# Kernel optimization log

Measured on AMD Instinct MI355X. Metric: run time of the kernel, lower is better.

Reference implementation:

```python
import jax, jax.numpy as jnp
import numpy as np

N_NODES = 50000
N_EDGES = 800000
IN_FT = 256
OUT_FT = 128


def setup_inputs() -> dict:
    key = jax.random.key(0)
    k_seq, k_src, k_dst, k_val, k_w = jax.random.split(key, 5)
    seq = jax.random.normal(k_seq, (N_NODES, IN_FT), dtype=jnp.float32)
    edge_src = jax.random.randint(k_src, (N_EDGES,), 0, N_NODES, dtype=jnp.int64)
    edge_dst = jax.random.randint(k_dst, (N_EDGES,), 0, N_NODES, dtype=jnp.int64)
    edge_val = jax.random.uniform(k_val, (N_EDGES,), dtype=jnp.float32)
    # xavier_uniform for Linear(in_ft, out_ft): limit = sqrt(6/(in+out))
    limit = float(np.sqrt(6.0 / (IN_FT + OUT_FT)))
    W = jax.random.uniform(k_w, (OUT_FT, IN_FT), minval=-limit, maxval=limit, dtype=jnp.float32)
    bias = jnp.zeros((OUT_FT,), dtype=jnp.float32)
    prelu_a = jnp.full((1,), 0.25, dtype=jnp.float32)  # nn.PReLU default slope
    return {"seq": seq, "edge_src": edge_src, "edge_dst": edge_dst,
            "edge_val": edge_val, "W": W, "bias": bias, "prelu_a": prelu_a}


def reference(seq, edge_src, edge_dst, edge_val, W, bias, prelu_a):
    # seq_fts = fc(seq): [N, out_ft]
    seq_fts = jnp.einsum('ni,oi->no', seq, W)
    # sparse spmm: out[dst] += val * seq_fts[src]
    msgs = seq_fts[edge_src] * edge_val[:, None]          # [E, out_ft]
    out = jax.ops.segment_sum(msgs, edge_dst, num_segments=seq.shape[0])
    out = out + bias                                       # bias add
    # PReLU with learnable slope a
    return jnp.where(out >= 0, out, prelu_a * out)
```

## Files before the change

kernel.cpp:

```cpp
#include <hip/hip_runtime.h>
#include <hip/hip_bf16.h>

#define N_NODES 50000
#define N_EDGES 800000
#define IN_FT 256
#define OUT_FT 128

typedef __bf16 bf16;
typedef __attribute__((ext_vector_type(8))) __bf16 bf16x8;
typedef __attribute__((ext_vector_type(4))) float floatx4;

static __device__ inline unsigned short f2bf_bits(float f) {
    unsigned u = __float_as_uint(f);
    return (unsigned short)((u + 0x7FFFu + ((u >> 16) & 1u)) >> 16);
}

__global__ __launch_bounds__(256) void k_wconv(const float* __restrict__ W,
                                               unsigned short* __restrict__ Wb) {
    int i = blockIdx.x * 256 + threadIdx.x;
    float4 v = ((const float4*)W)[i];
    ushort4 o;
    o.x = f2bf_bits(v.x); o.y = f2bf_bits(v.y);
    o.z = f2bf_bits(v.z); o.w = f2bf_bits(v.w);
    ((ushort4*)Wb)[i] = o;
}

#define WP 264
#define GM 128

__global__ __launch_bounds__(512) void k_gemm(const float* __restrict__ seq,
                                              const unsigned short* __restrict__ Wb,
                                              unsigned short* __restrict__ seq_fts) {
    __shared__ bf16 Wlds[128 * WP];
    const int t = threadIdx.x;

    {
        const int row = t >> 2, c0 = (t & 3) * 64;
        const unsigned short* src = Wb + row * IN_FT + c0;
        bf16* dst = Wlds + row * WP + c0;
#pragma unroll
        for (int c = 0; c < 8; ++c)
            *(uint4*)(dst + c * 8) = *(const uint4*)(src + c * 8);
    }

    const int lane = t & 63;
    const int wave = t >> 6;
    const int quad = lane >> 4;
    const int l16  = lane & 15;

    int arow = blockIdx.x * GM + wave * 16 + l16;
    if (arow >= N_NODES) arow = 0;
    const float* ap = seq + (size_t)arow * IN_FT + quad * 8;
    bf16x8 afr[8];
#pragma unroll
    for (int s = 0; s < 8; ++s) {
        float4 v0 = *(const float4*)(ap + s * 32);
        float4 v1 = *(const float4*)(ap + s * 32 + 4);
        bf16x8 a;
        a[0] = (bf16)v0.x; a[1] = (bf16)v0.y; a[2] = (bf16)v0.z; a[3] = (bf16)v0.w;
        a[4] = (bf16)v1.x; a[5] = (bf16)v1.y; a[6] = (bf16)v1.z; a[7] = (bf16)v1.w;
        afr[s] = a;
    }
    __syncthreads();

    const int mbase = blockIdx.x * GM + wave * 16;
#pragma unroll
    for (int tt = 0; tt < 8; ++tt) {
        floatx4 acc = {0.f, 0.f, 0.f, 0.f};
        const bf16* bp = Wlds + (tt * 16 + l16) * WP + quad * 8;
#pragma unroll
        for (int s = 0; s < 8; ++s) {
            bf16x8 bfr = *(const bf16x8*)(bp + s * 32);
            acc = __builtin_amdgcn_mfma_f32_16x16x32_bf16(afr[s], bfr, acc, 0, 0, 0);
        }
#pragma unroll
        for (int r = 0; r < 4; ++r) {
            int m = mbase + quad * 4 + r;
            if (m < N_NODES)
                seq_fts[(size_t)m * OUT_FT + tt * 16 + l16] = f2bf_bits(acc[r]);
        }
    }
}

#define P 256
#define CHUNK (N_EDGES / P)
#define NBUCK ((N_NODES + 255) / 256)
#define SCAN_B 256
#define NSCAN (NBUCK * P)
#define SNBLK (NSCAN / SCAN_B)

__global__ __launch_bounds__(256) void k_phist(const int* __restrict__ dst,
                                               int* __restrict__ cnt) {
    __shared__ int h[NBUCK];
    const int t = threadIdx.x;
    if (t < NBUCK) h[t] = 0;
    __syncthreads();
    const int base = blockIdx.x * CHUNK;
    for (int i = t; i < CHUNK; i += 256)
        atomicAdd(&h[dst[base + i] >> 8], 1);
    __syncthreads();
    if (t < NBUCK) cnt[t * P + blockIdx.x] = h[t];
}

__global__ __launch_bounds__(SCAN_B) void k_psum(const int* __restrict__ cnt,
                                                 int* __restrict__ part) {
    int i = blockIdx.x * SCAN_B + threadIdx.x;
    int v = cnt[i];
#pragma unroll
    for (int s = 32; s > 0; s >>= 1) v += __shfl_down(v, s, 64);
    __shared__ int w[4];
    if ((threadIdx.x & 63) == 0) w[threadIdx.x >> 6] = v;
    __syncthreads();
    if (threadIdx.x == 0) part[blockIdx.x] = w[0] + w[1] + w[2] + w[3];
}

__global__ __launch_bounds__(SCAN_B) void k_scanp(const int* __restrict__ part,
                                                  int* __restrict__ partoff) {
    __shared__ int lds[SCAN_B];
    int tid = threadIdx.x;
    int v = (tid < SNBLK) ? part[tid] : 0;
    lds[tid] = v;
    __syncthreads();
#pragma unroll
    for (int s = 1; s < SCAN_B; s <<= 1) {
        int t2 = (tid >= s) ? lds[tid - s] : 0;
        __syncthreads();
        lds[tid] += t2;
        __syncthreads();
    }
    if (tid < SNBLK) partoff[tid] = lds[tid] - v;
    if (tid == SCAN_B - 1) partoff[SNBLK] = lds[SCAN_B - 1];
}

__global__ __launch_bounds__(SCAN_B) void k_wrscan(const int* __restrict__ cnt,
                                                   const int* __restrict__ partoff,
                                                   int* __restrict__ cnt_off) {
    __shared__ int lds[SCAN_B];
    int tid = threadIdx.x;
    int i = blockIdx.x * SCAN_B + tid;
    int v = cnt[i];
    lds[tid] = v;
    __syncthreads();
#pragma unroll
    for (int s = 1; s < SCAN_B; s <<= 1) {
        int t2 = (tid >= s) ? lds[tid - s] : 0;
        __syncthreads();
        lds[tid] += t2;
        __syncthreads();
    }
    cnt_off[i] = partoff[blockIdx.x] + lds[tid] - v;
}

__global__ __launch_bounds__(256) void k_pscat(const int* __restrict__ src,
                                               const int* __restrict__ dst,
                                               const float* __restrict__ val,
                                               const int* __restrict__ cnt_off,
                                               uint2* __restrict__ part_ev) {
    __shared__ int off[NBUCK];
    const int t = threadIdx.x;
    if (t < NBUCK) off[t] = cnt_off[t * P + blockIdx.x];
    __syncthreads();
    const int base = blockIdx.x * CHUNK;
    for (int i = t; i < CHUNK; i += 256) {
        int e = base + i;
        int d = dst[e];
        int pos = atomicAdd(&off[d >> 8], 1);
        unsigned x = (unsigned)(unsigned short)src[e]
                   | ((unsigned)f2bf_bits(val[e]) << 16);
        part_ev[pos] = make_uint2(x, (unsigned)d);
    }
}

__global__ __launch_bounds__(256) void k_fill2(const uint2* __restrict__ part_ev,
                                               const int* __restrict__ partoff,
                                               int* __restrict__ row_ptr,
                                               unsigned* __restrict__ csr_ev) {
    __shared__ int cnt[256];
    __shared__ int lds[256];
    __shared__ int cur[256];
    const int b = blockIdx.x, t = threadIdx.x;
    const int start = partoff[b];
    const int end   = partoff[b + 1];
    cnt[t] = 0;
    __syncthreads();
    for (int i = start + t; i < end; i += 256)
        atomicAdd(&cnt[part_ev[i].y & 255u], 1);
    __syncthreads();
    int v = cnt[t];
    lds[t] = v;
    __syncthreads();
#pragma unroll
    for (int s = 1; s < 256; s <<= 1) {
        int t2 = (t >= s) ? lds[t - s] : 0;
        __syncthreads();
        lds[t] += t2;
        __syncthreads();
    }
    int base = start + lds[t] - v;
    int n = b * 256 + t;
    if (n <= N_NODES) row_ptr[n] = base;
    cur[t] = base;
    __syncthreads();
    for (int i = start + t; i < end; i += 256) {
        uint2 r = part_ev[i];
        int pos = atomicAdd(&cur[r.y & 255u], 1);
        csr_ev[pos] = r.x;
    }
}

#define GW 4
__global__ __launch_bounds__(64 * GW) void k_gather(const unsigned* __restrict__ fts,
                                                    const int* __restrict__ row_ptr,
                                                    const unsigned* __restrict__ csr_ev,
                                                    const float* __restrict__ bias,
                                                    const float* __restrict__ prelu_a,
                                                    float* __restrict__ out) {
    const int wave = threadIdx.x >> 6;
    const int lane = threadIdx.x & 63;
    const int n = blockIdx.x * GW + wave;
    if (n >= N_NODES) return;
    const int s0 = row_ptr[n];
    const int s1 = row_ptr[n + 1];
    float acc0 = 0.f, acc1 = 0.f;
    int j = s0;
    for (; j + 3 < s1; j += 4) {
        unsigned w0 = csr_ev[j],     w1 = csr_ev[j + 1];
        unsigned w2 = csr_ev[j + 2], w3 = csr_ev[j + 3];
        unsigned p0 = fts[(w0 & 0xFFFFu) * 64u + lane];
        unsigned p1 = fts[(w1 & 0xFFFFu) * 64u + lane];
        unsigned p2 = fts[(w2 & 0xFFFFu) * 64u + lane];
        unsigned p3 = fts[(w3 & 0xFFFFu) * 64u + lane];
        float v0 = __uint_as_float(w0 & 0xFFFF0000u);
        float v1 = __uint_as_float(w1 & 0xFFFF0000u);
        float v2 = __uint_as_float(w2 & 0xFFFF0000u);
        float v3 = __uint_as_float(w3 & 0xFFFF0000u);
        acc0 += v0 * __uint_as_float(p0 << 16);
        acc1 += v0 * __uint_as_float(p0 & 0xFFFF0000u);
        acc0 += v1 * __uint_as_float(p1 << 16);
        acc1 += v1 * __uint_as_float(p1 & 0xFFFF0000u);
        acc0 += v2 * __uint_as_float(p2 << 16);
        acc1 += v2 * __uint_as_float(p2 & 0xFFFF0000u);
        acc0 += v3 * __uint_as_float(p3 << 16);
        acc1 += v3 * __uint_as_float(p3 & 0xFFFF0000u);
    }
    for (; j < s1; ++j) {
        unsigned w0 = csr_ev[j];
        unsigned p0 = fts[(w0 & 0xFFFFu) * 64u + lane];
        float v0 = __uint_as_float(w0 & 0xFFFF0000u);
        acc0 += v0 * __uint_as_float(p0 << 16);
        acc1 += v0 * __uint_as_float(p0 & 0xFFFF0000u);
    }
    float2 b = *(const float2*)&bias[lane * 2];
    float a = prelu_a[0];
    float x0 = acc0 + b.x;
    float x1 = acc1 + b.y;
    x0 = (x0 >= 0.f) ? x0 : a * x0;
    x1 = (x1 >= 0.f) ? x1 : a * x1;
    *(float2*)&out[(size_t)n * OUT_FT + lane * 2] = make_float2(x0, x1);
}

extern "C" void kernel_launch(void* const* d_in, const int* in_sizes, int n_in,
                              void* d_out, int out_size, void* d_ws, size_t ws_size,
                              hipStream_t stream) {
    const float* seq      = (const float*)d_in[0];
    const int*   edge_src = (const int*)d_in[1];
    const int*   edge_dst = (const int*)d_in[2];
    const float* edge_val = (const float*)d_in[3];
    const float* W        = (const float*)d_in[4];
    const float* bias     = (const float*)d_in[5];
    const float* prelu_a  = (const float*)d_in[6];
    float* out = (float*)d_out;

    char* ws = (char*)d_ws;
    size_t off = 0;
    auto alloc = [&](size_t bytes) {
        void* p = ws + off;
        off = (off + bytes + 255) & ~(size_t)255;
        return p;
    };
    unsigned short* seq_fts = (unsigned short*)alloc((size_t)N_NODES * OUT_FT * sizeof(unsigned short));
    unsigned short* Wb      = (unsigned short*)alloc((size_t)OUT_FT * IN_FT * sizeof(unsigned short));
    int*   row_ptr = (int*)alloc((size_t)(N_NODES + 1) * sizeof(int));
    int*   cnt     = (int*)alloc((size_t)NSCAN * sizeof(int));
    int*   cnt_off = (int*)alloc((size_t)NSCAN * sizeof(int));
    int*   part    = (int*)alloc((size_t)SNBLK * sizeof(int));
    int*   partoff = (int*)alloc((size_t)(NBUCK + 1) * sizeof(int));
    uint2* part_ev = (uint2*)alloc((size_t)N_EDGES * sizeof(uint2));
    unsigned* csr_ev = (unsigned*)alloc((size_t)N_EDGES * sizeof(unsigned));
    (void)ws_size; (void)in_sizes; (void)n_in; (void)out_size;

    k_wconv<<<(OUT_FT * IN_FT / 4) / 256, 256, 0, stream>>>(W, Wb);
    k_gemm<<<(N_NODES + GM - 1) / GM, 512, 0, stream>>>(seq, Wb, seq_fts);
    k_phist<<<P, 256, 0, stream>>>(edge_dst, cnt);
    k_psum<<<SNBLK, SCAN_B, 0, stream>>>(cnt, part);
    k_scanp<<<1, SCAN_B, 0, stream>>>(part, partoff);
    k_wrscan<<<SNBLK, SCAN_B, 0, stream>>>(cnt, partoff, cnt_off);
    k_pscat<<<P, 256, 0, stream>>>(edge_src, edge_dst, edge_val, cnt_off, part_ev);
    k_fill2<<<NBUCK, 256, 0, stream>>>(part_ev, partoff, row_ptr, csr_ev);
    k_gather<<<(N_NODES + GW - 1) / GW, 64 * GW, 0, stream>>>((const unsigned*)seq_fts,
                                                              row_ptr, csr_ev,
                                                              bias, prelu_a, out);
}
```

Measured before the change: 187.2 us.

## Fuse prep kernels and merge GEMM with decoupled-lookback scan

Merges the weight conversion, histogram and status reset into one launch, and folds the three-kernel scan into the GEMM launch using extra blocks that run a single-pass decoupled-lookback scan with ticket ordering. This removes four kernel launches and lets the scan overlap with the GEMM. It adds spin-waiting on global status flags and 512-thread scan blocks in which half the threads sit idle. It also relies on forward progress of earlier-ticketed blocks.

```diff
diff --git a/kernel.cpp b/kernel.cpp
--- a/kernel.cpp
+++ b/kernel.cpp
@@ -15,140 +15,143 @@
     return (unsigned short)((u + 0x7FFFu + ((u >> 16) & 1u)) >> 16);
 }
 
-__global__ __launch_bounds__(256) void k_wconv(const float* __restrict__ W,
-                                               unsigned short* __restrict__ Wb) {
-    int i = blockIdx.x * 256 + threadIdx.x;
-    float4 v = ((const float4*)W)[i];
-    ushort4 o;
-    o.x = f2bf_bits(v.x); o.y = f2bf_bits(v.y);
-    o.z = f2bf_bits(v.z); o.w = f2bf_bits(v.w);
-    ((ushort4*)Wb)[i] = o;
-}
-
-#define WP 264
-#define GM 128
-
-__global__ __launch_bounds__(512) void k_gemm(const float* __restrict__ seq,
-                                              const unsigned short* __restrict__ Wb,
-                                              unsigned short* __restrict__ seq_fts) {
-    __shared__ bf16 Wlds[128 * WP];
-    const int t = threadIdx.x;
-
-    {
-        const int row = t >> 2, c0 = (t & 3) * 64;
-        const unsigned short* src = Wb + row * IN_FT + c0;
-        bf16* dst = Wlds + row * WP + c0;
-#pragma unroll
-        for (int c = 0; c < 8; ++c)
-            *(uint4*)(dst + c * 8) = *(const uint4*)(src + c * 8);
-    }
-
-    const int lane = t & 63;
-    const int wave = t >> 6;
-    const int quad = lane >> 4;
-    const int l16  = lane & 15;
-
-    int arow = blockIdx.x * GM + wave * 16 + l16;
-    if (arow >= N_NODES) arow = 0;
-    const float* ap = seq + (size_t)arow * IN_FT + quad * 8;
-    bf16x8 afr[8];
-#pragma unroll
-    for (int s = 0; s < 8; ++s) {
-        float4 v0 = *(const float4*)(ap + s * 32);
-        float4 v1 = *(const float4*)(ap + s * 32 + 4);
-        bf16x8 a;
-        a[0] = (bf16)v0.x; a[1] = (bf16)v0.y; a[2] = (bf16)v0.z; a[3] = (bf16)v0.w;
-        a[4] = (bf16)v1.x; a[5] = (bf16)v1.y; a[6] = (bf16)v1.z; a[7] = (bf16)v1.w;
-        afr[s] = a;
-    }
-    __syncthreads();
-
-    const int mbase = blockIdx.x * GM + wave * 16;
-#pragma unroll
-    for (int tt = 0; tt < 8; ++tt) {
-        floatx4 acc = {0.f, 0.f, 0.f, 0.f};
-        const bf16* bp = Wlds + (tt * 16 + l16) * WP + quad * 8;
-#pragma unroll
-        for (int s = 0; s < 8; ++s) {
-            bf16x8 bfr = *(const bf16x8*)(bp + s * 32);
-            acc = __builtin_amdgcn_mfma_f32_16x16x32_bf16(afr[s], bfr, acc, 0, 0, 0);
-        }
-#pragma unroll
-        for (int r = 0; r < 4; ++r) {
-            int m = mbase + quad * 4 + r;
-            if (m < N_NODES)
-                seq_fts[(size_t)m * OUT_FT + tt * 16 + l16] = f2bf_bits(acc[r]);
-        }
-    }
-}
-
 #define P 256
 #define CHUNK (N_EDGES / P)
 #define NBUCK ((N_NODES + 255) / 256)
-#define SCAN_B 256
 #define NSCAN (NBUCK * P)
-#define SNBLK (NSCAN / SCAN_B)
-
-__global__ __launch_bounds__(256) void k_phist(const int* __restrict__ dst,
-                                               int* __restrict__ cnt) {
-    __shared__ int h[NBUCK];
+#define GM 128
+#define GEMM_BLKS ((N_NODES + GM - 1) / GM)
+#define WP 264
+
+__global__ __launch_bounds__(256) void k_prep(const float* __restrict__ W,
+                                              const int* __restrict__ dst,
+                                              unsigned short* __restrict__ Wb,
+                                              int* __restrict__ cnt,
+                                              unsigned long long* __restrict__ status,
+                                              int* __restrict__ ticket) {
+    const int b = blockIdx.x, t = threadIdx.x;
+    if (b < P) {
+        __shared__ int h[NBUCK];
+        if (t < NBUCK) h[t] = 0;
+        __syncthreads();
+        const int base = b * CHUNK;
+        for (int i = t; i < CHUNK; i += 256)
+            atomicAdd(&h[dst[base + i] >> 8], 1);
+        __syncthreads();
+        if (t < NBUCK) cnt[t * P + b] = h[t];
+    } else if (b == P) {
+        if (t < NBUCK) status[t] = 0ull;
+        if (t == 255) *ticket = 0;
+    } else {
+        int i = (b - P - 1) * 256 + t;
+        float4 v = ((const float4*)W)[i];
+        ushort4 o;
+        o.x = f2bf_bits(v.x); o.y = f2bf_bits(v.y);
+        o.z = f2bf_bits(v.z); o.w = f2bf_bits(v.w);
+        ((ushort4*)Wb)[i] = o;
+    }
+}
+
+__global__ __launch_bounds__(512) void k_gemm_scan(const float* __restrict__ seq,
+                                                   const unsigned short* __restrict__ Wb,
+                                                   unsigned short* __restrict__ seq_fts,
+                                                   const int* __restrict__ cnt,
+                                                   int* __restrict__ cnt_off,
+                                                   int* __restrict__ partoff,
+                                                   unsigned long long* __restrict__ status,
+                                                   int* __restrict__ ticket) {
     const int t = threadIdx.x;
-    if (t < NBUCK) h[t] = 0;
-    __syncthreads();
-    const int base = blockIdx.x * CHUNK;
-    for (int i = t; i < CHUNK; i += 256)
-        atomicAdd(&h[dst[base + i] >> 8], 1);
-    __syncthreads();
-    if (t < NBUCK) cnt[t * P + blockIdx.x] = h[t];
-}
-
-__global__ __launch_bounds__(SCAN_B) void k_psum(const int* __restrict__ cnt,
-                                                 int* __restrict__ part) {
-    int i = blockIdx.x * SCAN_B + threadIdx.x;
-    int v = cnt[i];
-#pragma unroll
-    for (int s = 32; s > 0; s >>= 1) v += __shfl_down(v, s, 64);
-    __shared__ int w[4];
-    if ((threadIdx.x & 63) == 0) w[threadIdx.x >> 6] = v;
-    __syncthreads();
-    if (threadIdx.x == 0) part[blockIdx.x] = w[0] + w[1] + w[2] + w[3];
-}
-
-__global__ __launch_bounds__(SCAN_B) void k_scanp(const int* __restrict__ part,
-                                                  int* __restrict__ partoff) {
-    __shared__ int lds[SCAN_B];
-    int tid = threadIdx.x;
-    int v = (tid < SNBLK) ? part[tid] : 0;
-    lds[tid] = v;
-    __syncthreads();
-#pragma unroll
-    for (int s = 1; s < SCAN_B; s <<= 1) {
-        int t2 = (tid >= s) ? lds[tid - s] : 0;
-        __syncthreads();
-        lds[tid] += t2;
-        __syncthreads();
-    }
-    if (tid < SNBLK) partoff[tid] = lds[tid] - v;
-    if (tid == SCAN_B - 1) partoff[SNBLK] = lds[SCAN_B - 1];
-}
-
-__global__ __launch_bounds__(SCAN_B) void k_wrscan(const int* __restrict__ cnt,
-                                                   const int* __restrict__ partoff,
-                                                   int* __restrict__ cnt_off) {
-    __shared__ int lds[SCAN_B];
-    int tid = threadIdx.x;
-    int i = blockIdx.x * SCAN_B + tid;
-    int v = cnt[i];
-    lds[tid] = v;
-    __syncthreads();
-#pragma unroll
-    for (int s = 1; s < SCAN_B; s <<= 1) {
-        int t2 = (tid >= s) ? lds[tid - s] : 0;
-        __syncthreads();
-        lds[tid] += t2;
-        __syncthreads();
-    }
-    cnt_off[i] = partoff[blockIdx.x] + lds[tid] - v;
+    if (blockIdx.x < GEMM_BLKS) {
+        __shared__ bf16 Wlds[128 * WP];
+        {
+            const int row = t >> 2, c0 = (t & 3) * 64;
+            const unsigned short* src = Wb + row * IN_FT + c0;
+            bf16* dstp = Wlds + row * WP + c0;
+#pragma unroll
+            for (int c = 0; c < 8; ++c)
+                *(uint4*)(dstp + c * 8) = *(const uint4*)(src + c * 8);
+        }
+        const int lane = t & 63;
+        const int wave = t >> 6;
+        const int quad = lane >> 4;
+        const int l16  = lane & 15;
+
+        int arow = blockIdx.x * GM + wave * 16 + l16;
+        if (arow >= N_NODES) arow = 0;
+        const float* ap = seq + (size_t)arow * IN_FT + quad * 8;
+        bf16x8 afr[8];
+#pragma unroll
+        for (int s = 0; s < 8; ++s) {
+            float4 v0 = *(const float4*)(ap + s * 32);
+            float4 v1 = *(const float4*)(ap + s * 32 + 4);
+            bf16x8 a;
+            a[0] = (bf16)v0.x; a[1] = (bf16)v0.y; a[2] = (bf16)v0.z; a[3] = (bf16)v0.w;
+            a[4] = (bf16)v1.x; a[5] = (bf16)v1.y; a[6] = (bf16)v1.z; a[7] = (bf16)v1.w;
+            afr[s] = a;
+        }
+        __syncthreads();
+
+        const int mbase = blockIdx.x * GM + wave * 16;
+#pragma unroll
+        for (int tt = 0; tt < 8; ++tt) {
+            floatx4 acc = {0.f, 0.f, 0.f, 0.f};
+            const bf16* bp = Wlds + (tt * 16 + l16) * WP + quad * 8;
+#pragma unroll
+            for (int s = 0; s < 8; ++s) {
+                bf16x8 bfr = *(const bf16x8*)(bp + s * 32);
+                acc = __builtin_amdgcn_mfma_f32_16x16x32_bf16(afr[s], bfr, acc, 0, 0, 0);
+            }
+#pragma unroll
+            for (int r = 0; r < 4; ++r) {
+                int m = mbase + quad * 4 + r;
+                if (m < N_NODES)
+                    seq_fts[(size_t)m * OUT_FT + tt * 16 + l16] = f2bf_bits(acc[r]);
+            }
+        }
+    } else {
+        __shared__ int lds2[256];
+        __shared__ int stile;
+        __shared__ unsigned run_sh;
+        if (t == 0) stile = atomicAdd(ticket, 1);
+        __syncthreads();
+        const int j = stile;
+        int v = (t < 256) ? cnt[j * 256 + t] : 0;
+        if (t < 256) lds2[t] = v;
+        __syncthreads();
+        for (int s = 1; s < 256; s <<= 1) {
+            int add = (t < 256 && t >= s) ? lds2[t - s] : 0;
+            __syncthreads();
+            if (t < 256) lds2[t] += add;
+            __syncthreads();
+        }
+        const unsigned total = (unsigned)lds2[255];
+        if (t == 0) {
+            if (j == 0) {
+                atomicExch(&status[0], ((unsigned long long)total << 2) | 2ull);
+                run_sh = 0;
+            } else {
+                atomicExch(&status[j], ((unsigned long long)total << 2) | 1ull);
+                unsigned running = 0;
+                int k = j - 1;
+                for (;;) {
+                    unsigned long long s = atomicAdd(&status[k], 0ull);
+                    unsigned st = (unsigned)(s & 3ull);
+                    if (st == 0u) { __builtin_amdgcn_s_sleep(1); continue; }
+                    running += (unsigned)(s >> 2);
+                    if (st == 2u) break;
+                    --k;
+                }
+                atomicExch(&status[j],
+                           ((unsigned long long)(running + total) << 2) | 2ull);
+                run_sh = running;
+            }
+        }
+        __syncthreads();
+        const int base = (int)run_sh;
+        if (t < 256) cnt_off[j * 256 + t] = base + lds2[t] - v;
+        if (t == 0) partoff[j] = base;
+        if (t == 0 && j == NBUCK - 1) partoff[NBUCK] = base + (int)total;
+    }
 }
 
 __global__ __launch_bounds__(256) void k_pscat(const int* __restrict__ src,
@@ -283,18 +286,16 @@
     int*   row_ptr = (int*)alloc((size_t)(N_NODES + 1) * sizeof(int));
     int*   cnt     = (int*)alloc((size_t)NSCAN * sizeof(int));
     int*   cnt_off = (int*)alloc((size_t)NSCAN * sizeof(int));
-    int*   part    = (int*)alloc((size_t)SNBLK * sizeof(int));
     int*   partoff = (int*)alloc((size_t)(NBUCK + 1) * sizeof(int));
+    unsigned long long* status = (unsigned long long*)alloc((size_t)NBUCK * sizeof(unsigned long long));
+    int*   ticket  = (int*)alloc(256);
     uint2* part_ev = (uint2*)alloc((size_t)N_EDGES * sizeof(uint2));
     unsigned* csr_ev = (unsigned*)alloc((size_t)N_EDGES * sizeof(unsigned));
     (void)ws_size; (void)in_sizes; (void)n_in; (void)out_size;
 
-    k_wconv<<<(OUT_FT * IN_FT / 4) / 256, 256, 0, stream>>>(W, Wb);
-    k_gemm<<<(N_NODES + GM - 1) / GM, 512, 0, stream>>>(seq, Wb, seq_fts);
-    k_phist<<<P, 256, 0, stream>>>(edge_dst, cnt);
-    k_psum<<<SNBLK, SCAN_B, 0, stream>>>(cnt, part);
-    k_scanp<<<1, SCAN_B, 0, stream>>>(part, partoff);
-    k_wrscan<<<SNBLK, SCAN_B, 0, stream>>>(cnt, partoff, cnt_off);
+    k_prep<<<P + 1 + 32, 256, 0, stream>>>(W, edge_dst, Wb, cnt, status, ticket);
+    k_gemm_scan<<<GEMM_BLKS + NBUCK, 512, 0, stream>>>(seq, Wb, seq_fts, cnt,
+                                                       cnt_off, partoff, status, ticket);
     k_pscat<<<P, 256, 0, stream>>>(edge_src, edge_dst, edge_val, cnt_off, part_ev);
     k_fill2<<<NBUCK, 256, 0, stream>>>(part_ev, partoff, row_ptr, csr_ev);
     k_gather<<<(N_NODES + GW - 1) / GW, 64 * GW, 0, stream>>>((const unsigned*)seq_fts,
```

Result: faster. 181.0 us (median of 2 runs) (-3.3%).
